# Kernel tuning notes

Measured on AMD Instinct MI355X. Metric: run time of the kernel, lower is better.

The kernel has to match this reference:

```python
import jax, jax.numpy as jnp
import numpy as np

RESIZE = 518   # image_encoder.resize_size (DINOv2)
PATCH = 14     # image_encoder.patch_size
GRID = RESIZE // PATCH          # 37
TOTAL = GRID * GRID             # 1369


def setup_inputs() -> dict:
    key = jax.random.key(0)
    ks = jax.random.split(key, 10)
    B, C, V, D, F, P = 2, 6, 50000, 384, 64, 100000
    M = TOTAL
    patch_tokens = jax.random.normal(ks[0], (B, C, M, D), jnp.float32)
    voxel_features = jax.random.normal(ks[1], (B, V, F), jnp.float32)
    voxel_coords = jax.random.normal(ks[2], (B, V, 3), jnp.float32) * 20.0
    image_sizes = jnp.tile(jnp.array([[900.0, 1600.0]], jnp.float32), (B, 1))
    # realistic pinhole intrinsics (fx=fy=1200, cx=800, cy=450)
    K = jnp.array([[1200.0, 0.0, 800.0], [0.0, 1200.0, 450.0], [0.0, 0.0, 1.0]], jnp.float32)
    cam_intrinsics = jnp.broadcast_to(K, (B, C, 3, 3))
    # extrinsics: identity rotation + random translation per camera
    Rt = jnp.broadcast_to(jnp.eye(4, dtype=jnp.float32), (B, C, 4, 4))
    t = jax.random.normal(ks[3], (B, C, 3), jnp.float32) * 5.0
    lidar2cam_extrinsics = Rt.at[..., :3, 3].set(t)
    point2voxel_idx = jax.random.randint(ks[4], (B, P), 0, V)
    W1 = jax.random.normal(ks[5], (F + D, 256), jnp.float32) * 0.02
    b1 = jnp.zeros((256,), jnp.float32)
    W2 = jax.random.normal(ks[6], (256, 64), jnp.float32) * 0.02
    b2 = jnp.zeros((64,), jnp.float32)
    W3 = jax.random.normal(ks[7], (64, 16), jnp.float32) * 0.02
    b3 = jnp.zeros((16,), jnp.float32)
    return {"patch_tokens": patch_tokens, "voxel_features": voxel_features,
            "voxel_coords": voxel_coords, "image_sizes": image_sizes,
            "cam_intrinsics": cam_intrinsics, "lidar2cam_extrinsics": lidar2cam_extrinsics,
            "point2voxel_idx": point2voxel_idx,
            "W1": W1, "b1": b1, "W2": W2, "b2": b2, "W3": W3, "b3": b3}


def reference(patch_tokens, voxel_features, voxel_coords, image_sizes,
              cam_intrinsics, lidar2cam_extrinsics, point2voxel_idx,
              W1, b1, W2, b2, W3, b3):
    B, V, _ = voxel_coords.shape
    # ---- multi_camera_projector, vectorized over cameras ----
    pts_h = jnp.concatenate([voxel_coords, jnp.ones((B, V, 1), voxel_coords.dtype)], -1)
    cam_pts = jnp.einsum('bcij,bvj->bcvi', lidar2cam_extrinsics, pts_h)  # (B,C,V,4)
    xyz = cam_pts[..., :3]
    z = xyz[..., 2]
    pix = jnp.einsum('bcij,bcvj->bcvi', cam_intrinsics, xyz)             # (B,C,V,3)
    denom = jnp.maximum(pix[..., 2], 1e-12)
    u = pix[..., 0] / denom
    v = pix[..., 1] / denom
    H = image_sizes[:, 0][:, None, None]
    W = image_sizes[:, 1][:, None, None]
    valid = (z > 0) & (u >= 0) & (u < W) & (v >= 0) & (v < H)            # (B,C,V)
    coords = jnp.where(valid[..., None], jnp.stack([u, v], -1), -1.0)    # (B,C,V,2)
    # ---- scale_pixel_coords to (RESIZE, RESIZE) ----
    scale = jnp.stack([RESIZE / jnp.maximum(image_sizes[:, 1], 1e-6),
                       RESIZE / jnp.maximum(image_sizes[:, 0], 1e-6)], -1)  # (B,2) = (sw, sh)
    coords = coords * scale[:, None, None, :]
    # ---- patch grid indexing (trunc-toward-zero like torch .long()) ----
    pxy = (coords / float(PATCH)).astype(jnp.int32)
    px = jnp.clip(pxy[..., 0], 0, GRID - 1)
    py = jnp.clip(pxy[..., 1], 0, GRID - 1)
    flat = jnp.clip(py * GRID + px, 0, TOTAL - 1)                        # (B,C,V)
    gathered = jnp.take_along_axis(patch_tokens, flat[..., None], axis=2)  # (B,C,V,D)
    # ---- masked mean over cameras ----
    mask = valid[..., None].astype(patch_tokens.dtype)
    fused_img = (gathered * mask).sum(1) / jnp.maximum(mask.sum(1), 1.0)  # (B,V,D)
    # ---- concat + MLP ----
    fused = jnp.concatenate([voxel_features, fused_img], -1)             # (B,V,F+D)
    h = jax.nn.relu(fused @ W1 + b1)
    h = jax.nn.relu(h @ W2 + b2)
    voxel_scores = h @ W3 + b3                                           # (B,V,16)
    # ---- devoxelize: gather voxel scores back to points ----
    point_scores = jnp.take_along_axis(voxel_scores, point2voxel_idx[..., None], axis=1)
    return point_scores
```

## Files before the change

### kernel.cpp

```cpp
#include <hip/hip_runtime.h>

#define NB 2
#define NC 6
#define NV 50000
#define ND 384
#define NF 64
#define NP 100000
#define NM 1369
#define NROW (NB*NV)
#define NT (NB*NC*NM)
#define TILE 32

typedef __attribute__((ext_vector_type(8))) short bf8_t;
typedef __attribute__((ext_vector_type(4))) float f4_t;

__device__ inline unsigned short f2bf(float x) {
    unsigned u = __builtin_bit_cast(unsigned, x);
    u += 0x7fffu + ((u >> 16) & 1u);
    return (unsigned short)(u >> 16);
}
__device__ inline unsigned pack2bf(float lo, float hi) {
    return (unsigned)f2bf(lo) | ((unsigned)f2bf(hi) << 16);
}
__device__ inline float bflo(unsigned u) { return __builtin_bit_cast(float, u << 16); }
__device__ inline float bfhi(unsigned u) { return __builtin_bit_cast(float, u & 0xffff0000u); }

__device__ inline void proj_one(const float* __restrict__ E,
                                const float* __restrict__ Km,
                                float x, float y, float z,
                                float Ws, float Hs, float sx, float sy,
                                bool& valid, int& flat)
{
#pragma clang fp contract(off)
    const float X = ((E[0]*x + E[1]*y) + E[2]*z) + E[3];
    const float Y = ((E[4]*x + E[5]*y) + E[6]*z) + E[7];
    const float Z = ((E[8]*x + E[9]*y) + E[10]*z) + E[11];
    const float p0 = (Km[0]*X + Km[1]*Y) + Km[2]*Z;
    const float p1 = (Km[3]*X + Km[4]*Y) + Km[5]*Z;
    const float p2 = (Km[6]*X + Km[7]*Y) + Km[8]*Z;
    const float den = fmaxf(p2, 1e-12f);
    const float u = p0 / den;
    const float v = p1 / den;
    valid = (Z > 0.0f) & (u >= 0.0f) & (u < Ws) & (v >= 0.0f) & (v < Hs);
    const float us = u * sx;
    const float vs = v * sy;
    int px = (int)(us / 14.0f);
    int py = (int)(vs / 14.0f);
    px = px < 0 ? 0 : (px > 36 ? 36 : px);
    py = py < 0 ? 0 : (py > 36 ? 36 : py);
    flat = py*37 + px;
}

__global__ __launch_bounds__(256) void pack_all(
    const float* __restrict__ W1, const float* __restrict__ W2,
    const float* __restrict__ W3,
    unsigned short* __restrict__ o1, unsigned short* __restrict__ o2,
    unsigned short* __restrict__ o3)
{
    const int blk = blockIdx.x;
    if (blk < 448) {
        const int t = blk*256 + threadIdx.x;
        const int k = t >> 8, n = t & 255;
        const int kc = k >> 5, g = (k >> 3) & 3, i = k & 7;
        const int w = n >> 6, nf = (n >> 4) & 3, m = n & 15;
        o1[(((kc*16 + w*4 + nf)*64 + g*16 + m) << 3) + i] = f2bf(W1[k*256 + n]);
    } else if (blk < 512) {
        const int t = (blk - 448)*256 + threadIdx.x;
        const int k = t >> 6, n = t & 63;
        const int kc = k >> 5, g = (k >> 3) & 3, i = k & 7;
        const int nf = n >> 4, m = n & 15;
        o2[(((kc*4 + nf)*64 + g*16 + m) << 3) + i] = f2bf(W2[k*64 + n]);
    } else {
        const int t = (blk - 512)*256 + threadIdx.x;
        const int k = t >> 4, n = t & 15;
        const int kc = k >> 5, g = (k >> 3) & 3, i = k & 7;
        o3[((kc*64 + g*16 + n) << 3) + i] = f2bf(W3[k*16 + n]);
    }
}

__global__ __launch_bounds__(256) void ptok_kernel(
    const float* __restrict__ patch,
    const unsigned short* __restrict__ w1p_,
    unsigned short* __restrict__ T)
{
    __shared__ __align__(16) unsigned short sA[32*408];

    const int tid  = threadIdx.x;
    const int lane = tid & 63;
    const int w    = tid >> 6;
    const int mrow = lane & 15;
    const int kg   = lane >> 4;
    const int rbase = blockIdx.x * 32;

    unsigned* sA32 = (unsigned*)sA;
    #pragma unroll
    for (int i = 0; i < 8; ++i) {
        const int r = w + 4*i;
        int row = rbase + r;
        row = row < NT ? row : NT - 1;
        const float2* src = (const float2*)(patch + (size_t)row*ND);
        #pragma unroll
        for (int c = 0; c < 3; ++c) {
            const float2 v = src[c*64 + lane];
            sA32[r*204 + c*64 + lane] = pack2bf(v.x, v.y);
        }
    }
    __syncthreads();

    const bf8_t* w1p = (const bf8_t*)w1p_;
    const f4_t zero = {0.f, 0.f, 0.f, 0.f};
    f4_t acc[2][4];
    #pragma unroll
    for (int a = 0; a < 2; ++a)
        #pragma unroll
        for (int q = 0; q < 4; ++q) acc[a][q] = zero;

    for (int j = 0; j < 12; ++j) {
        const bf8_t a0 = *(const bf8_t*)&sA[ mrow      *408 + j*32 + kg*8];
        const bf8_t a1 = *(const bf8_t*)&sA[(mrow + 16)*408 + j*32 + kg*8];
        const bf8_t* bp = w1p + (size_t)(((j+2)*16 + w*4)*64 + lane);
        #pragma unroll
        for (int nf = 0; nf < 4; ++nf) {
            const bf8_t bfr = bp[nf*64];
            acc[0][nf] = __builtin_amdgcn_mfma_f32_16x16x32_bf16(a0, bfr, acc[0][nf], 0, 0, 0);
            acc[1][nf] = __builtin_amdgcn_mfma_f32_16x16x32_bf16(a1, bfr, acc[1][nf], 0, 0, 0);
        }
    }
    #pragma unroll
    for (int nf = 0; nf < 4; ++nf)
        #pragma unroll
        for (int mf = 0; mf < 2; ++mf)
            #pragma unroll
            for (int r = 0; r < 4; ++r) {
                const int trow = rbase + mf*16 + kg*4 + r;
                if (trow < NT)
                    T[(size_t)trow*256 + w*64 + nf*16 + mrow] = f2bf(acc[mf][nf][r]);
            }
}

__global__ __launch_bounds__(256, 7) void fuse_mlp_kernel(
    const float* __restrict__ vfeat,
    const float* __restrict__ vcoord,
    const float* __restrict__ imsz,
    const float* __restrict__ intr,
    const float* __restrict__ extr,
    const float* __restrict__ b1,
    const float* __restrict__ b2,
    const float* __restrict__ b3,
    const unsigned short* __restrict__ w1p_,
    const unsigned short* __restrict__ w2p_,
    const unsigned short* __restrict__ w3p_,
    const unsigned short* __restrict__ T,
    float* __restrict__ scores)
{
    __shared__ __align__(16) unsigned short sVP[TILE*264];
    __shared__ __align__(16) unsigned short sVF[TILE*72];
    __shared__ int sFlat[NC*TILE];

    const int tid  = threadIdx.x;
    const int base = blockIdx.x * TILE;
    const int lane = tid & 63;
    const int w    = tid >> 6;
    const int mrow = lane & 15;
    const int kg   = lane >> 4;

    #pragma unroll
    for (int i = 0; i < 8; ++i) {
        const int e = tid + 256*i;
        const int r = e >> 6, c = e & 63;
        sVF[r*72 + c] = f2bf(vfeat[(size_t)(base + r)*NF + c]);
    }

    if (tid < NC*TILE) {
        const int r = tid & 31, c = tid >> 5;
        const int n = base + r;
        const int b = n / NV;
        const float x = vcoord[(size_t)n*3+0];
        const float y = vcoord[(size_t)n*3+1];
        const float z = vcoord[(size_t)n*3+2];
        const float Hs = imsz[b*2+0];
        const float Ws = imsz[b*2+1];
        const float sx = 518.0f / fmaxf(Ws, 1e-6f);
        const float sy = 518.0f / fmaxf(Hs, 1e-6f);
        const float* E  = extr + (size_t)(b*NC + c)*16;
        const float* Km = intr + (size_t)(b*NC + c)*9;
        bool valid; int flat;
        proj_one(E, Km, x, y, z, Ws, Hs, sx, sy, valid, flat);
        sFlat[c*TILE + r] = valid ? flat : -1;
    }
    __syncthreads();

    const bf8_t* w1p = (const bf8_t*)w1p_;
    const f4_t zero = {0.f, 0.f, 0.f, 0.f};
    f4_t acc1[2][4];
    #pragma unroll
    for (int a = 0; a < 2; ++a)
        #pragma unroll
        for (int q = 0; q < 4; ++q) acc1[a][q] = zero;
    #pragma unroll
    for (int kc = 0; kc < 2; ++kc) {
        const bf8_t a0 = *(const bf8_t*)&sVF[ mrow      *72 + kc*32 + kg*8];
        const bf8_t a1 = *(const bf8_t*)&sVF[(mrow + 16)*72 + kc*32 + kg*8];
        const bf8_t* bp = w1p + (size_t)((kc*16 + w*4)*64 + lane);
        #pragma unroll
        for (int nf = 0; nf < 4; ++nf) {
            const bf8_t bfr = bp[nf*64];
            acc1[0][nf] = __builtin_amdgcn_mfma_f32_16x16x32_bf16(a0, bfr, acc1[0][nf], 0, 0, 0);
            acc1[1][nf] = __builtin_amdgcn_mfma_f32_16x16x32_bf16(a1, bfr, acc1[1][nf], 0, 0, 0);
        }
    }
    #pragma unroll
    for (int nf = 0; nf < 4; ++nf) {
        const float bb = b1[w*64 + nf*16 + mrow];
        #pragma unroll
        for (int mf = 0; mf < 2; ++mf)
            #pragma unroll
            for (int r = 0; r < 4; ++r)
                sVP[(mf*16 + kg*4 + r)*264 + w*64 + nf*16 + mrow] = f2bf(acc1[mf][nf][r] + bb);
    }
    __syncthreads();

    #pragma unroll
    for (int t4 = 0; t4 < 4; ++t4) {
        const int r0 = w + 8*t4, r1 = r0 + 4;
        const int b0 = (base + r0) / NV, b1v = (base + r1) / NV;
        float g00=0.f,g01=0.f,g02=0.f,g03=0.f; int cnt0 = 0;
        float g10=0.f,g11=0.f,g12=0.f,g13=0.f; int cnt1 = 0;
        #pragma unroll
        for (int c = 0; c < NC; ++c) {
            const int f0 = sFlat[c*TILE + r0];
            const int f1 = sFlat[c*TILE + r1];
            if (f0 >= 0) {
                const uint2 u = *(const uint2*)(T + ((size_t)((b0*NC + c)*NM + f0))*256 + lane*4);
                g00 += bflo(u.x); g01 += bfhi(u.x);
                g02 += bflo(u.y); g03 += bfhi(u.y);
                ++cnt0;
            }
            if (f1 >= 0) {
                const uint2 u = *(const uint2*)(T + ((size_t)((b1v*NC + c)*NM + f1))*256 + lane*4);
                g10 += bflo(u.x); g11 += bfhi(u.x);
                g12 += bflo(u.y); g13 += bfhi(u.y);
                ++cnt1;
            }
        }
        const float inv0 = 1.0f / fmaxf((float)cnt0, 1.0f);
        const float inv1 = 1.0f / fmaxf((float)cnt1, 1.0f);
        {
            uint2 vp = *(uint2*)&sVP[r0*264 + lane*4];
            const float h0 = fmaxf(g00*inv0 + bflo(vp.x), 0.f);
            const float h1v = fmaxf(g01*inv0 + bfhi(vp.x), 0.f);
            const float h2v = fmaxf(g02*inv0 + bflo(vp.y), 0.f);
            const float h3 = fmaxf(g03*inv0 + bfhi(vp.y), 0.f);
            uint2 o; o.x = pack2bf(h0, h1v); o.y = pack2bf(h2v, h3);
            *(uint2*)&sVP[r0*264 + lane*4] = o;
        }
        {
            uint2 vp = *(uint2*)&sVP[r1*264 + lane*4];
            const float h0 = fmaxf(g10*inv1 + bflo(vp.x), 0.f);
            const float h1v = fmaxf(g11*inv1 + bfhi(vp.x), 0.f);
            const float h2v = fmaxf(g12*inv1 + bflo(vp.y), 0.f);
            const float h3 = fmaxf(g13*inv1 + bfhi(vp.y), 0.f);
            uint2 o; o.x = pack2bf(h0, h1v); o.y = pack2bf(h2v, h3);
            *(uint2*)&sVP[r1*264 + lane*4] = o;
        }
    }
    __syncthreads();

    unsigned short* sH1 = sVP;
    unsigned short* sH2bf = sVF;
    const bf8_t* w2p = (const bf8_t*)w2p_;
    f4_t acc2[2];
    acc2[0] = zero; acc2[1] = zero;
    for (int kc = 0; kc < 8; ++kc) {
        const bf8_t a0 = *(const bf8_t*)&sH1[ mrow      *264 + kc*32 + kg*8];
        const bf8_t a1 = *(const bf8_t*)&sH1[(mrow + 16)*264 + kc*32 + kg*8];
        const bf8_t bfr = w2p[(kc*4 + w)*64 + lane];
        acc2[0] = __builtin_amdgcn_mfma_f32_16x16x32_bf16(a0, bfr, acc2[0], 0, 0, 0);
        acc2[1] = __builtin_amdgcn_mfma_f32_16x16x32_bf16(a1, bfr, acc2[1], 0, 0, 0);
    }
    {
        const float bb = b2[w*16 + mrow];
        #pragma unroll
        for (int mf = 0; mf < 2; ++mf)
            #pragma unroll
            for (int r = 0; r < 4; ++r) {
                const float v = fmaxf(acc2[mf][r] + bb, 0.f);
                sH2bf[(mf*16 + kg*4 + r)*72 + w*16 + mrow] = f2bf(v);
            }
    }
    __syncthreads();

    if (w < 2) {
        const bf8_t* w3p = (const bf8_t*)w3p_;
        f4_t acc3 = zero;
        #pragma unroll
        for (int kc = 0; kc < 2; ++kc) {
            const bf8_t a = *(const bf8_t*)&sH2bf[(w*16 + mrow)*72 + kc*32 + kg*8];
            const bf8_t bfr = w3p[kc*64 + lane];
            acc3 = __builtin_amdgcn_mfma_f32_16x16x32_bf16(a, bfr, acc3, 0, 0, 0);
        }
        const float bb = b3[mrow];
        #pragma unroll
        for (int r = 0; r < 4; ++r)
            scores[(size_t)(base + w*16 + kg*4 + r)*16 + mrow] = acc3[r] + bb;
    }
}

__global__ __launch_bounds__(256) void gather_kernel(
    const float* __restrict__ scores,
    const int* __restrict__ p2v,
    float* __restrict__ out)
{
    const int g  = blockIdx.x * 256 + threadIdx.x;
    const int q  = g & 3;
    const int pl = g >> 2;
    const int b  = pl / NP;
    const int idx = p2v[pl];
    const float4 val = *(const float4*)&scores[((size_t)(b*NV + idx))*16 + q*4];
    *(float4*)&out[(size_t)g*4] = val;
}

extern "C" void kernel_launch(void* const* d_in, const int* in_sizes, int n_in,
                              void* d_out, int out_size, void* d_ws, size_t ws_size,
                              hipStream_t stream) {
    const float* patch = (const float*)d_in[0];
    const float* vfeat = (const float*)d_in[1];
    const float* vcoord= (const float*)d_in[2];
    const float* imsz  = (const float*)d_in[3];
    const float* intr  = (const float*)d_in[4];
    const float* extr  = (const float*)d_in[5];
    const int*   p2v   = (const int*)d_in[6];
    const float* W1 = (const float*)d_in[7];
    const float* b1 = (const float*)d_in[8];
    const float* W2 = (const float*)d_in[9];
    const float* b2 = (const float*)d_in[10];
    const float* W3 = (const float*)d_in[11];
    const float* b3 = (const float*)d_in[12];

    float* scores = (float*)d_ws;
    unsigned short* w1pack = (unsigned short*)((char*)d_ws + 6400000);
    unsigned short* w2pack = (unsigned short*)((char*)d_ws + 6629376);
    unsigned short* w3pack = (unsigned short*)((char*)d_ws + 6662144);
    unsigned short* Tbuf   = (unsigned short*)((char*)d_ws + 6664192);

    pack_all<<<516, 256, 0, stream>>>(W1, W2, W3, w1pack, w2pack, w3pack);
    ptok_kernel<<<(NT + 31)/32, 256, 0, stream>>>(patch, w1pack, Tbuf);
    fuse_mlp_kernel<<<NROW/TILE, 256, 0, stream>>>(
        vfeat, vcoord, imsz, intr, extr,
        b1, b2, b3, w1pack, w2pack, w3pack, Tbuf, scores);
    gather_kernel<<<(NB*NP*4)/256, 256, 0, stream>>>(scores, p2v, (float*)d_out);
}
```

Measured before the change: 58.74 us.

## Software-pipeline gather loads of projected tokens and vectorize voxel feature staging

Issues the gather loads for the first row's six camera tokens before the first-layer MFMA, then double-buffers the gathers so each row's loads are issued one iteration ahead. Loads become unconditional, with invalid cameras clamped to index 0 and masked in the sum, so memory latency overlaps with compute. Voxel features are now loaded as float2 and packed into bf16 pairs. Launch bounds drop from 7 to 6 blocks per CU to make room for the extra registers, which may reduce occupancy, and the unconditional loads add some wasted traffic for invalid cameras.

```diff
diff --git a/kernel.cpp b/kernel.cpp
--- a/kernel.cpp
+++ b/kernel.cpp
@@ -138,7 +138,7 @@
             }
 }
 
-__global__ __launch_bounds__(256, 7) void fuse_mlp_kernel(
+__global__ __launch_bounds__(256, 6) void fuse_mlp_kernel(
     const float* __restrict__ vfeat,
     const float* __restrict__ vcoord,
     const float* __restrict__ imsz,
@@ -165,10 +165,11 @@
     const int kg   = lane >> 4;
 
     #pragma unroll
-    for (int i = 0; i < 8; ++i) {
+    for (int i = 0; i < 4; ++i) {
         const int e = tid + 256*i;
-        const int r = e >> 6, c = e & 63;
-        sVF[r*72 + c] = f2bf(vfeat[(size_t)(base + r)*NF + c]);
+        const int r = e >> 5, c2 = e & 31;
+        const float2 v = *(const float2*)&vfeat[(size_t)(base + r)*NF + c2*2];
+        *(unsigned*)&sVF[r*72 + c2*2] = pack2bf(v.x, v.y);
     }
 
     if (tid < NC*TILE) {
@@ -190,6 +191,20 @@
     }
     __syncthreads();
 
+    uint2 buf[2][NC];
+    int   fl[2][NC];
+    {
+        const int r0 = w;
+        const int b0 = (base + r0) / NV;
+        #pragma unroll
+        for (int c = 0; c < NC; ++c) {
+            const int f = sFlat[c*TILE + r0];
+            fl[0][c] = f;
+            const int fc = f < 0 ? 0 : f;
+            buf[0][c] = *(const uint2*)(T + ((size_t)((b0*NC + c)*NM + fc))*256 + lane*4);
+        }
+    }
+
     const bf8_t* w1p = (const bf8_t*)w1p_;
     const f4_t zero = {0.f, 0.f, 0.f, 0.f};
     f4_t acc1[2][4];
@@ -221,48 +236,39 @@
     __syncthreads();
 
     #pragma unroll
-    for (int t4 = 0; t4 < 4; ++t4) {
-        const int r0 = w + 8*t4, r1 = r0 + 4;
-        const int b0 = (base + r0) / NV, b1v = (base + r1) / NV;
-        float g00=0.f,g01=0.f,g02=0.f,g03=0.f; int cnt0 = 0;
-        float g10=0.f,g11=0.f,g12=0.f,g13=0.f; int cnt1 = 0;
+    for (int t = 0; t < 8; ++t) {
+        if (t < 7) {
+            const int rn = w + 4*(t+1);
+            const int bn = (base + rn) / NV;
+            #pragma unroll
+            for (int c = 0; c < NC; ++c) {
+                const int f = sFlat[c*TILE + rn];
+                fl[(t+1)&1][c] = f;
+                const int fc = f < 0 ? 0 : f;
+                buf[(t+1)&1][c] = *(const uint2*)(T + ((size_t)((bn*NC + c)*NM + fc))*256 + lane*4);
+            }
+        }
+        const int r = w + 4*t;
+        float g0=0.f, g1=0.f, g2=0.f, g3=0.f;
+        int cnt = 0;
         #pragma unroll
         for (int c = 0; c < NC; ++c) {
-            const int f0 = sFlat[c*TILE + r0];
-            const int f1 = sFlat[c*TILE + r1];
-            if (f0 >= 0) {
-                const uint2 u = *(const uint2*)(T + ((size_t)((b0*NC + c)*NM + f0))*256 + lane*4);
-                g00 += bflo(u.x); g01 += bfhi(u.x);
-                g02 += bflo(u.y); g03 += bfhi(u.y);
-                ++cnt0;
-            }
-            if (f1 >= 0) {
-                const uint2 u = *(const uint2*)(T + ((size_t)((b1v*NC + c)*NM + f1))*256 + lane*4);
-                g10 += bflo(u.x); g11 += bfhi(u.x);
-                g12 += bflo(u.y); g13 += bfhi(u.y);
-                ++cnt1;
-            }
-        }
-        const float inv0 = 1.0f / fmaxf((float)cnt0, 1.0f);
-        const float inv1 = 1.0f / fmaxf((float)cnt1, 1.0f);
-        {
-            uint2 vp = *(uint2*)&sVP[r0*264 + lane*4];
-            const float h0 = fmaxf(g00*inv0 + bflo(vp.x), 0.f);
-            const float h1v = fmaxf(g01*inv0 + bfhi(vp.x), 0.f);
-            const float h2v = fmaxf(g02*inv0 + bflo(vp.y), 0.f);
-            const float h3 = fmaxf(g03*inv0 + bfhi(vp.y), 0.f);
-            uint2 o; o.x = pack2bf(h0, h1v); o.y = pack2bf(h2v, h3);
-            *(uint2*)&sVP[r0*264 + lane*4] = o;
-        }
-        {
-            uint2 vp = *(uint2*)&sVP[r1*264 + lane*4];
-            const float h0 = fmaxf(g10*inv1 + bflo(vp.x), 0.f);
-            const float h1v = fmaxf(g11*inv1 + bfhi(vp.x), 0.f);
-            const float h2v = fmaxf(g12*inv1 + bflo(vp.y), 0.f);
-            const float h3 = fmaxf(g13*inv1 + bfhi(vp.y), 0.f);
-            uint2 o; o.x = pack2bf(h0, h1v); o.y = pack2bf(h2v, h3);
-            *(uint2*)&sVP[r1*264 + lane*4] = o;
-        }
+            const bool v = fl[t&1][c] >= 0;
+            const uint2 u = buf[t&1][c];
+            g0 += v ? bflo(u.x) : 0.f;
+            g1 += v ? bfhi(u.x) : 0.f;
+            g2 += v ? bflo(u.y) : 0.f;
+            g3 += v ? bfhi(u.y) : 0.f;
+            cnt += v ? 1 : 0;
+        }
+        const float inv = 1.0f / fmaxf((float)cnt, 1.0f);
+        uint2 vp = *(uint2*)&sVP[r*264 + lane*4];
+        const float h0 = fmaxf(g0*inv + bflo(vp.x), 0.f);
+        const float h1v = fmaxf(g1*inv + bfhi(vp.x), 0.f);
+        const float h2v = fmaxf(g2*inv + bflo(vp.y), 0.f);
+        const float h3 = fmaxf(g3*inv + bfhi(vp.y), 0.f);
+        uint2 o; o.x = pack2bf(h0, h1v); o.y = pack2bf(h2v, h3);
+        *(uint2*)&sVP[r*264 + lane*4] = o;
     }
     __syncthreads();
 
```

Result: slower. 67.70 us (+15.3%).
